# Performance work log

Hardware: AMD Instinct MI355X
Metric: run time of the kernel (lower is better)

Reference implementation:

```python
import jax, jax.numpy as jnp
import numpy as np

N_NODES = 200   # sensors
SEQ = 128       # sequence_length == d_model of per-node transformers
BATCH = 256     # transformer treats batch as the attention sequence (2D input)
HEADS = 4
LAYERS = 2
NF = 1          # num_features (forced to 1 by fc dims)
F_OUT = 64      # num_out_features
G_OUT = 64      # gnn_output_dim
N_EDGES = 1600
D = SEQ
EPS = 1e-5


def setup_inputs() -> dict:
    key = jax.random.key(0)
    ks = jax.random.split(key, 20)
    s = 0.05
    nrm = lambda k, shp: jax.random.normal(k, shp, jnp.float32) * s
    return {
        "x": jax.random.normal(ks[0], (BATCH, N_NODES, SEQ), jnp.float32),
        "edge_index": jax.random.randint(ks[1], (2, N_EDGES), 0, N_NODES),
        # per-node, per-layer transformer params (stacked for vmap)
        "Wqkv": nrm(ks[2], (N_NODES, LAYERS, 3 * D, D)),
        "bqkv": nrm(ks[3], (N_NODES, LAYERS, 3 * D)),
        "Wo": nrm(ks[4], (N_NODES, LAYERS, D, D)),
        "bo": nrm(ks[5], (N_NODES, LAYERS, D)),
        "g1": jnp.ones((N_NODES, LAYERS, D), jnp.float32),
        "be1": jnp.zeros((N_NODES, LAYERS, D), jnp.float32),
        "fW1": nrm(ks[6], (N_NODES, LAYERS, D, D)),  # dim_feedforward = SEQ = D
        "fb1": nrm(ks[7], (N_NODES, LAYERS, D)),
        "fW2": nrm(ks[8], (N_NODES, LAYERS, D, D)),
        "fb2": nrm(ks[9], (N_NODES, LAYERS, D)),
        "g2": jnp.ones((N_NODES, LAYERS, D), jnp.float32),
        "be2": jnp.zeros((N_NODES, LAYERS, D), jnp.float32),
        # shared fc: Linear(SEQ*NF, F_OUT)
        "fc_W": nrm(ks[10], (F_OUT, SEQ * NF)),
        "fc_b": nrm(ks[11], (F_OUT,)),
        # GATConv(F_OUT, G_OUT), heads=1
        "gat_W": nrm(ks[12], (G_OUT, F_OUT)),
        "att_src": nrm(ks[13], (G_OUT,)),
        "att_dst": nrm(ks[14], (G_OUT,)),
        "gat_b": nrm(ks[15], (G_OUT,)),
        # predictor Linear(G_OUT, 2)
        "pred_W": nrm(ks[16], (2, G_OUT)),
        "pred_b": nrm(ks[17], (2,)),
    }


def _ln(v, g, b):
    m = v.mean(-1, keepdims=True)
    var = ((v - m) ** 2).mean(-1, keepdims=True)
    return (v - m) / jnp.sqrt(var + EPS) * g + b


def _encoder_one_node(xn, Wqkv, bqkv, Wo, bo, g1, be1, fW1, fb1, fW2, fb2, g2, be2):
    # xn: [S, D] with S = BATCH (torch treats the 2D input as unbatched seq)
    dh = D // HEADS
    scale = jnp.asarray(1.0 / np.sqrt(dh), xn.dtype)
    for l in range(LAYERS):  # post-norm TransformerEncoderLayer, relu, no dropout (eval)
        qkv = xn @ Wqkv[l].T + bqkv[l]                    # [S, 3D]
        q, k, v = jnp.split(qkv, 3, axis=-1)
        q = q.reshape(-1, HEADS, dh)
        k = k.reshape(-1, HEADS, dh)
        v = v.reshape(-1, HEADS, dh)
        s = jnp.einsum('qhd,khd->hqk', q, k) * scale      # [H, S, S]
        a = jax.nn.softmax(s, axis=-1)
        o = jnp.einsum('hqk,khd->qhd', a, v).reshape(-1, D)
        o = o @ Wo[l].T + bo[l]
        xn = _ln(xn + o, g1[l], be1[l])
        f = jax.nn.relu(xn @ fW1[l].T + fb1[l]) @ fW2[l].T + fb2[l]
        xn = _ln(xn + f, g2[l], be2[l])
    return xn


def _forward(edge_index, x, Wqkv, bqkv, Wo, bo, g1, be1, fW1, fb1, fW2, fb2, g2, be2,
             fc_W, fc_b, gat_W, att_src, att_dst, gat_b, pred_W, pred_b):
    B, N, _ = x.shape
    xt = jnp.transpose(x, (1, 0, 2))                      # [N, B, D]
    t_out = jax.vmap(_encoder_one_node)(xt, Wqkv, bqkv, Wo, bo, g1, be1,
                                        fW1, fb1, fW2, fb2, g2, be2)  # [N, B, D]
    feat = t_out @ fc_W.T + fc_b                          # [N, B, F_OUT]
    # replicate torch.cat(dim=0) over nodes followed by .view(B, N, F)
    feat = feat.reshape(N * B, F_OUT).reshape(B, N, F_OUT)

    # GATConv with add_self_loops, heads=1, negative_slope=0.2
    loops = jnp.arange(N, dtype=edge_index.dtype)
    src = jnp.concatenate([edge_index[0], loops])
    dst = jnp.concatenate([edge_index[1], loops])

    def gat(h_in):  # h_in: [N, F_OUT]
        h = h_in @ gat_W.T                                # [N, G_OUT]
        a_s = h @ att_src                                 # [N]
        a_d = h @ att_dst
        e = jax.nn.leaky_relu(a_s[src] + a_d[dst], 0.2)   # [E+N]
        emax = jax.ops.segment_max(e, dst, num_segments=N)
        emax = jnp.where(jnp.isfinite(emax), emax, 0.0)
        w = jnp.exp(e - emax[dst])
        denom = jax.ops.segment_sum(w, dst, num_segments=N)
        alpha = w / (denom[dst] + 1e-16)
        return jax.ops.segment_sum(alpha[:, None] * h[src], dst, num_segments=N) + gat_b

    g = jax.vmap(gat)(feat)                               # [B, N, G_OUT]
    return g @ pred_W.T + pred_b                          # [B, N, 2]


def reference(x, edge_index, Wqkv, bqkv, Wo, bo, g1, be1, fW1, fb1, fW2, fb2, g2, be2,
              fc_W, fc_b, gat_W, att_src, att_dst, gat_b, pred_W, pred_b):
    return _forward(edge_index, x, Wqkv, bqkv, Wo, bo, g1, be1, fW1, fb1, fW2, fb2,
                    g2, be2, fc_W, fc_b, gat_W, att_src, att_dst, gat_b, pred_W, pred_b)
```

## Files before the change

### kernel.cpp

```cpp
#include <hip/hip_runtime.h>
#include <hip/hip_bf16.h>

#define NN 200
#define BB 256
#define DD 128
#define DH 32
#define NE 1600
#define LL 2

typedef short short8 __attribute__((ext_vector_type(8)));
typedef short short4a __attribute__((ext_vector_type(4)));
typedef float floatx4 __attribute__((ext_vector_type(4)));
using bf16 = __hip_bfloat16;

__device__ __forceinline__ short bfs(float x) {
  bf16 h = __float2bfloat16(x);
  return *(short*)&h;
}
__device__ __forceinline__ float b2f(short s) {
  union { unsigned u; float f; } cv;
  cv.u = ((unsigned)(unsigned short)s) << 16;
  return cv.f;
}

__device__ __forceinline__ void swz_node(int bid, int per_node, int& node, int& rem) {
  int xcd = bid & 7;
  int slot = bid >> 3;
  int q = slot / per_node;
  node = xcd * (NN >> 3) + q;
  rem = slot - q * per_node;
}

__device__ __forceinline__ void ldw_regs(const float* __restrict__ wbase, int tid,
                                         float4* vr) {
#pragma unroll
  for (int i = 0; i < 8; i++) vr[i] = *(const float4*)(wbase + (i * 256 + tid) * 4);
}
__device__ __forceinline__ void st_ws(const float4* vr, short* WS, int tid) {
#pragma unroll
  for (int i = 0; i < 8; i++) {
    int idx = i * 256 + tid;
    int rw = idx >> 5, k = (idx & 31) << 2;
    short4a p = {bfs(vr[i].x), bfs(vr[i].y), bfs(vr[i].z), bfs(vr[i].w)};
    *(short4a*)&WS[rw * 136 + k] = p;
  }
}
__device__ __forceinline__ void stage_w(const float* __restrict__ wbase,
                                        short* WS, int tid) {
  float4 vr[8];
  ldw_regs(wbase, tid, vr);
  st_ws(vr, WS, tid);
}

__device__ __forceinline__ void gemm_q(const short8* af, const short* WS, int r,
                                       int quad, floatx4* acc) {
#pragma unroll
  for (int k0 = 0; k0 < 4; k0++) {
#pragma unroll
    for (int s = 0; s < 4; s++) {
      short8 bq = *(const short8*)&WS[(s * 16 + r) * 136 + quad * 8 + k0 * 32];
      acc[s] = __builtin_amdgcn_mfma_f32_16x16x32_bf16(af[k0], bq, acc[s], 0, 0, 0);
    }
  }
}

__global__ __launch_bounds__(256) void k_transpose(const float* __restrict__ x,
                                                   bf16* __restrict__ X) {
  int tid = blockIdx.x * 256 + threadIdx.x;
  if (tid >= NN * BB * DD) return;
  int d = tid & (DD - 1);
  int rest = tid >> 7;
  int b = rest & (BB - 1);
  int node = rest >> 8;
  X[tid] = (bf16)x[((size_t)b * NN + node) * DD + d];
}

template <int MTPW>
__global__ __launch_bounds__(256) void k_gemm64(const bf16* __restrict__ A,
                                                const float* __restrict__ W,
                                                const float* __restrict__ bias,
                                                bf16* __restrict__ out, int nout,
                                                int astride, size_t woff, int wns,
                                                size_t boff, int bns, int relu,
                                                int nc_count) {
  __shared__ short WS[64 * 136];
  const int RSPLIT = 4 / MTPW;
  int per_node = nc_count * RSPLIT;
  int node, rem;
  swz_node(blockIdx.x, per_node, node, rem);
  int nc = rem / RSPLIT;
  int rh = rem - nc * RSPLIT;
  int tid = threadIdx.x;
  int w = tid >> 6, lane = tid & 63, r = lane & 15, quad = lane >> 4;
  int base_row = rh * 128 + w * (MTPW * 16);

  short8 areg[MTPW][4];
#pragma unroll
  for (int mt = 0; mt < MTPW; mt++) {
    const bf16* arow =
        A + ((size_t)node * BB + base_row + mt * 16 + r) * (size_t)astride + quad * 8;
#pragma unroll
    for (int k = 0; k < 4; k++) areg[mt][k] = *(const short8*)(arow + k * 32);
  }

  stage_w(W + woff + (size_t)node * (size_t)wns + (size_t)nc * 64 * DD, WS, tid);
  __syncthreads();

  floatx4 acc[MTPW][4];
  floatx4 z = {0.f, 0.f, 0.f, 0.f};
#pragma unroll
  for (int mt = 0; mt < MTPW; mt++)
#pragma unroll
    for (int s = 0; s < 4; s++) acc[mt][s] = z;

#pragma unroll
  for (int k0 = 0; k0 < 4; k0++) {
    short8 bq[4];
#pragma unroll
    for (int s = 0; s < 4; s++)
      bq[s] = *(const short8*)&WS[(s * 16 + r) * 136 + quad * 8 + k0 * 32];
#pragma unroll
    for (int mt = 0; mt < MTPW; mt++)
#pragma unroll
      for (int s = 0; s < 4; s++)
        acc[mt][s] = __builtin_amdgcn_mfma_f32_16x16x32_bf16(areg[mt][k0], bq[s],
                                                             acc[mt][s], 0, 0, 0);
  }

  const float* bp = bias + boff + (size_t)node * (size_t)bns + nc * 64;
  float bv[4];
#pragma unroll
  for (int s = 0; s < 4; s++) bv[s] = bp[s * 16 + r];

  __syncthreads();
  short* mybw = &WS[w * 1088];
  const size_t obase = (size_t)node * BB + base_row;
#pragma unroll
  for (int mt = 0; mt < MTPW; mt++) {
#pragma unroll
    for (int s = 0; s < 4; s++) {
#pragma unroll
      for (int i = 0; i < 4; i++) {
        float v = acc[mt][s][i] + bv[s];
        if (relu) v = v > 0.f ? v : 0.f;
        mybw[(quad * 4 + i) * 68 + s * 16 + r] = bfs(v);
      }
    }
#pragma unroll
    for (int j = 0; j < 2; j++) {
      int chunk = j * 64 + lane;
      int rowr = chunk >> 3, c8 = chunk & 7;
      short8 o = *(const short8*)&mybw[rowr * 68 + c8 * 8];
      *(short8*)((short*)out + (obase + mt * 16 + rowr) * (size_t)nout + nc * 64 + c8 * 8) = o;
    }
  }
}

__global__ __launch_bounds__(256) void k_ffn(const bf16* __restrict__ QKV,
                                             const float* __restrict__ Wo,
                                             const float* __restrict__ bo,
                                             bf16* __restrict__ X,
                                             const float* __restrict__ g1,
                                             const float* __restrict__ be1,
                                             const float* __restrict__ fW1,
                                             const float* __restrict__ fb1,
                                             const float* __restrict__ fW2,
                                             const float* __restrict__ fb2,
                                             const float* __restrict__ g2,
                                             const float* __restrict__ be2,
                                             size_t wso, int wns, size_t bso, int bns,
                                             int gstride,
                                             const float* __restrict__ W4,
                                             const float* __restrict__ C4,
                                             float* __restrict__ AS,
                                             float* __restrict__ ADv,
                                             float* __restrict__ HW0,
                                             float* __restrict__ HW1,
                                             int dofinal) {
  __shared__ short WS[64 * 136];
  __shared__ short HB[64 * 136];
  __shared__ short FB[64 * 136];
  int node, bt;
  swz_node(blockIdx.x, 4, node, bt);
  int tid = threadIdx.x;
  int w = tid >> 6, lane = tid & 63, r = lane & 15, quad = lane >> 4;
  int rrow = lane >> 2, cg = lane & 3;
  int row0 = bt * 64 + w * 16;

  const short* qrow = (const short*)QKV + ((size_t)node * BB + row0 + r) * 384 + quad * 8;
  short8 af[4];
#pragma unroll
  for (int k0 = 0; k0 < 4; k0++) af[k0] = *(const short8*)(qrow + k0 * 32);
  size_t xoff = ((size_t)node * BB + row0 + rrow) * DD + cg * 32;
  short8 xres[4];
#pragma unroll
  for (int c = 0; c < 4; c++) xres[c] = *(const short8*)((const short*)X + xoff + c * 8);

  const float* WoN = Wo + wso + (size_t)node * (size_t)wns;
  const float* W1N = fW1 + wso + (size_t)node * (size_t)wns;
  const float* W2N = fW2 + wso + (size_t)node * (size_t)wns;

  floatx4 z = {0.f, 0.f, 0.f, 0.f};
  floatx4 acc[8];
  float vv[32];
  float bv[8];
  float4 wreg[8];

  ldw_regs(WoN, tid, wreg);
  st_ws(wreg, WS, tid);
  __syncthreads();
  ldw_regs(WoN + 64 * DD, tid, wreg);
#pragma unroll
  for (int s = 0; s < 8; s++) acc[s] = z;
  gemm_q(af, WS, r, quad, &acc[0]);
  __syncthreads();
  st_ws(wreg, WS, tid);
  __syncthreads();
  ldw_regs(W1N, tid, wreg);
  gemm_q(af, WS, r, quad, &acc[4]);

  const float* bpo = bo + bso + (size_t)node * (size_t)bns;
#pragma unroll
  for (int cch = 0; cch < 2; cch++)
#pragma unroll
    for (int s = 0; s < 4; s++) bv[cch * 4 + s] = bpo[cch * 64 + s * 16 + r];

  {
    float* BNC = (float*)&HB[w * 16 * 136];
#pragma unroll
    for (int s = 0; s < 4; s++)
#pragma unroll
      for (int i = 0; i < 4; i++)
        BNC[(quad * 4 + i) * 68 + s * 16 + r] = acc[s][i] + bv[s];
    if (cg < 2) {
#pragma unroll
      for (int j = 0; j < 8; j++) {
        float4 t4 = *(const float4*)&BNC[rrow * 68 + (cg & 1) * 32 + j * 4];
        vv[j * 4 + 0] = t4.x; vv[j * 4 + 1] = t4.y;
        vv[j * 4 + 2] = t4.z; vv[j * 4 + 3] = t4.w;
      }
    }
#pragma unroll
    for (int s = 0; s < 4; s++)
#pragma unroll
      for (int i = 0; i < 4; i++)
        BNC[(quad * 4 + i) * 68 + s * 16 + r] = acc[4 + s][i] + bv[4 + s];
    if (cg >= 2) {
#pragma unroll
      for (int j = 0; j < 8; j++) {
        float4 t4 = *(const float4*)&BNC[rrow * 68 + (cg & 1) * 32 + j * 4];
        vv[j * 4 + 0] = t4.x; vv[j * 4 + 1] = t4.y;
        vv[j * 4 + 2] = t4.z; vv[j * 4 + 3] = t4.w;
      }
    }
  }

  float sum = 0.f;
#pragma unroll
  for (int c = 0; c < 4; c++)
#pragma unroll
    for (int j = 0; j < 8; j++) {
      vv[c * 8 + j] += b2f(xres[c][j]);
      sum += vv[c * 8 + j];
    }
  sum += __shfl_xor(sum, 1);
  sum += __shfl_xor(sum, 2);
  float mean = sum * (1.0f / 128.0f);
  float vs = 0.f;
#pragma unroll
  for (int j = 0; j < 32; j++) {
    float d = vv[j] - mean;
    vs += d * d;
  }
  vs += __shfl_xor(vs, 1);
  vs += __shfl_xor(vs, 2);
  float inv = rsqrtf(vs * (1.0f / 128.0f) + 1e-5f);
  {
    const float* gp = g1 + bso + (size_t)node * gstride + cg * 32;
    const float* bep = be1 + bso + (size_t)node * gstride + cg * 32;
#pragma unroll
    for (int c = 0; c < 8; c++) {
      float4 g4 = *(const float4*)(gp + c * 4);
      float4 b4 = *(const float4*)(bep + c * 4);
      vv[c * 4 + 0] = (vv[c * 4 + 0] - mean) * inv * g4.x + b4.x;
      vv[c * 4 + 1] = (vv[c * 4 + 1] - mean) * inv * g4.y + b4.y;
      vv[c * 4 + 2] = (vv[c * 4 + 2] - mean) * inv * g4.z + b4.z;
      vv[c * 4 + 3] = (vv[c * 4 + 3] - mean) * inv * g4.w + b4.w;
    }
  }
  {
    short* hrow = &HB[(w * 16 + rrow) * 136 + cg * 32];
#pragma unroll
    for (int c = 0; c < 4; c++) {
      short8 hs;
#pragma unroll
      for (int j = 0; j < 8; j++) hs[j] = bfs(vv[c * 8 + j]);
      *(short8*)(hrow + c * 8) = hs;
    }
  }

  __syncthreads();
  st_ws(wreg, WS, tid);
  __syncthreads();
  ldw_regs(W1N + 64 * DD, tid, wreg);
  short8 hf[4];
#pragma unroll
  for (int k0 = 0; k0 < 4; k0++)
    hf[k0] = *(const short8*)&HB[(w * 16 + r) * 136 + quad * 8 + k0 * 32];
#pragma unroll
  for (int s = 0; s < 8; s++) acc[s] = z;
  gemm_q(hf, WS, r, quad, &acc[0]);
  __syncthreads();
  st_ws(wreg, WS, tid);
  __syncthreads();
  ldw_regs(W2N, tid, wreg);
  gemm_q(hf, WS, r, quad, &acc[4]);
  {
    const float* bp1 = fb1 + bso + (size_t)node * (size_t)bns;
#pragma unroll
    for (int cch = 0; cch < 2; cch++)
#pragma unroll
      for (int s = 0; s < 4; s++) {
        float bb = bp1[cch * 64 + s * 16 + r];
#pragma unroll
        for (int i = 0; i < 4; i++) {
          float v2 = acc[cch * 4 + s][i] + bb;
          FB[(w * 16 + quad * 4 + i) * 136 + cch * 64 + s * 16 + r] =
              bfs(v2 > 0.f ? v2 : 0.f);
        }
      }
  }

  __syncthreads();
  st_ws(wreg, WS, tid);
  __syncthreads();
  ldw_regs(W2N + 64 * DD, tid, wreg);
  short8 ff[4];
#pragma unroll
  for (int k0 = 0; k0 < 4; k0++)
    ff[k0] = *(const short8*)&FB[(w * 16 + r) * 136 + quad * 8 + k0 * 32];
#pragma unroll
  for (int s = 0; s < 8; s++) acc[s] = z;
  gemm_q(ff, WS, r, quad, &acc[0]);
  __syncthreads();
  st_ws(wreg, WS, tid);
  __syncthreads();
  gemm_q(ff, WS, r, quad, &acc[4]);

  const float* bp2 = fb2 + bso + (size_t)node * (size_t)bns;
#pragma unroll
  for (int cch = 0; cch < 2; cch++)
#pragma unroll
    for (int s = 0; s < 4; s++) bv[cch * 4 + s] = bp2[cch * 64 + s * 16 + r];

  {
    float* BNC = (float*)&FB[w * 16 * 136];
#pragma unroll
    for (int s = 0; s < 4; s++)
#pragma unroll
      for (int i = 0; i < 4; i++)
        BNC[(quad * 4 + i) * 68 + s * 16 + r] = acc[s][i] + bv[s];
    if (cg < 2) {
#pragma unroll
      for (int j = 0; j < 8; j++) {
        float4 t4 = *(const float4*)&BNC[rrow * 68 + (cg & 1) * 32 + j * 4];
        vv[j * 4 + 0] = t4.x; vv[j * 4 + 1] = t4.y;
        vv[j * 4 + 2] = t4.z; vv[j * 4 + 3] = t4.w;
      }
    }
#pragma unroll
    for (int s = 0; s < 4; s++)
#pragma unroll
      for (int i = 0; i < 4; i++)
        BNC[(quad * 4 + i) * 68 + s * 16 + r] = acc[4 + s][i] + bv[4 + s];
    if (cg >= 2) {
#pragma unroll
      for (int j = 0; j < 8; j++) {
        float4 t4 = *(const float4*)&BNC[rrow * 68 + (cg & 1) * 32 + j * 4];
        vv[j * 4 + 0] = t4.x; vv[j * 4 + 1] = t4.y;
        vv[j * 4 + 2] = t4.z; vv[j * 4 + 3] = t4.w;
      }
    }
  }

  sum = 0.f;
#pragma unroll
  for (int c = 0; c < 4; c++) {
    short8 hs = *(const short8*)&HB[(w * 16 + rrow) * 136 + cg * 32 + c * 8];
#pragma unroll
    for (int j = 0; j < 8; j++) {
      vv[c * 8 + j] += b2f(hs[j]);
      sum += vv[c * 8 + j];
    }
  }
  sum += __shfl_xor(sum, 1);
  sum += __shfl_xor(sum, 2);
  mean = sum * (1.0f / 128.0f);
  vs = 0.f;
#pragma unroll
  for (int j = 0; j < 32; j++) {
    float d = vv[j] - mean;
    vs += d * d;
  }
  vs += __shfl_xor(vs, 1);
  vs += __shfl_xor(vs, 2);
  inv = rsqrtf(vs * (1.0f / 128.0f) + 1e-5f);
  {
    const float* gp = g2 + bso + (size_t)node * gstride + cg * 32;
    const float* bep = be2 + bso + (size_t)node * gstride + cg * 32;
#pragma unroll
    for (int c = 0; c < 8; c++) {
      float4 g4 = *(const float4*)(gp + c * 4);
      float4 b4 = *(const float4*)(bep + c * 4);
      vv[c * 4 + 0] = (vv[c * 4 + 0] - mean) * inv * g4.x + b4.x;
      vv[c * 4 + 1] = (vv[c * 4 + 1] - mean) * inv * g4.y + b4.y;
      vv[c * 4 + 2] = (vv[c * 4 + 2] - mean) * inv * g4.z + b4.z;
      vv[c * 4 + 3] = (vv[c * 4 + 3] - mean) * inv * g4.w + b4.w;
    }
  }

  if (!dofinal) {
#pragma unroll
    for (int c = 0; c < 4; c++) {
      short8 os;
#pragma unroll
      for (int j = 0; j < 8; j++) os[j] = bfs(vv[c * 8 + j]);
      *(short8*)((short*)X + xoff + c * 8) = os;
    }
  } else {
    float a0 = 0.f, a1 = 0.f, a2 = 0.f, a3 = 0.f;
#pragma unroll
    for (int c = 0; c < 8; c++) {
      float4 w0 = *(const float4*)(W4 + cg * 32 + c * 4);
      float4 w1 = *(const float4*)(W4 + 128 + cg * 32 + c * 4);
      float4 w2 = *(const float4*)(W4 + 256 + cg * 32 + c * 4);
      float4 w3 = *(const float4*)(W4 + 384 + cg * 32 + c * 4);
      a0 += vv[c * 4] * w0.x + vv[c * 4 + 1] * w0.y + vv[c * 4 + 2] * w0.z + vv[c * 4 + 3] * w0.w;
      a1 += vv[c * 4] * w1.x + vv[c * 4 + 1] * w1.y + vv[c * 4 + 2] * w1.z + vv[c * 4 + 3] * w1.w;
      a2 += vv[c * 4] * w2.x + vv[c * 4 + 1] * w2.y + vv[c * 4 + 2] * w2.z + vv[c * 4 + 3] * w2.w;
      a3 += vv[c * 4] * w3.x + vv[c * 4 + 1] * w3.y + vv[c * 4 + 2] * w3.z + vv[c * 4 + 3] * w3.w;
    }
    a0 += __shfl_xor(a0, 1); a0 += __shfl_xor(a0, 2);
    a1 += __shfl_xor(a1, 1); a1 += __shfl_xor(a1, 2);
    a2 += __shfl_xor(a2, 1); a2 += __shfl_xor(a2, 2);
    a3 += __shfl_xor(a3, 1); a3 += __shfl_xor(a3, 2);
    if (cg == 0) {
      int grow = node * BB + row0 + rrow;
      AS[grow] = a0 + C4[0];
      ADv[grow] = a1 + C4[1];
      HW0[grow] = a2 + C4[2];
      HW1[grow] = a3 + C4[3];
    }
  }
}

__global__ __launch_bounds__(256) void k_attn(bf16* __restrict__ QKV) {
  __shared__ short VT[32 * 264];
  __shared__ short Pw[4 * 2560];
  int node, h;
  swz_node(blockIdx.x, 4, node, h);
  int tid = threadIdx.x;
  int wave = tid >> 6, lane = tid & 63, quad = lane >> 4, l15 = lane & 15;
  short* sbase = (short*)(QKV + (size_t)node * BB * 384);

  int q0 = wave * 64;
  short8 qf[4];
#pragma unroll
  for (int qt = 0; qt < 4; qt++)
    qf[qt] = *(const short8*)(sbase + (size_t)(q0 + qt * 16 + l15) * 384 + h * 32 + quad * 8);

#pragma unroll
  for (int it = 0; it < 4; it++) {
    int i = it * 256 + tid;
    int key = i >> 2, dq = (i & 3) << 3;
    short8 v8 = *(const short8*)(sbase + (size_t)key * 384 + 256 + h * 32 + dq);
#pragma unroll
    for (int j = 0; j < 8; j++) VT[(dq + j) * 264 + key] = v8[j];
  }
  __syncthreads();

  floatx4 zz = {0.f, 0.f, 0.f, 0.f};
  floatx4 acc[2][4];
#pragma unroll
  for (int dt = 0; dt < 2; dt++)
#pragma unroll
    for (int qt = 0; qt < 4; qt++) acc[dt][qt] = zz;
  float lp[4] = {0.f, 0.f, 0.f, 0.f};
  const float scale = 0.17677669529663689f;
  short* mypw = &Pw[wave * 2560];

#define KADDR(kt) (const short8*)(sbase + (size_t)((kt) * 16 + l15) * 384 + 128 + h * 32 + quad * 8)
  short8 kfA = *KADDR(0);
  short8 kfB = *KADDR(1);

  for (int g = 0; g < 8; g++) {
    short8 vf0 = *(const short8*)(&VT[l15 * 264 + g * 32 + quad * 8]);
    short8 vf1 = *(const short8*)(&VT[(16 + l15) * 264 + g * 32 + quad * 8]);
    short8 nA = kfA, nB = kfB;
    if (g < 7) {
      nA = *KADDR(g * 2 + 2);
      nB = *KADDR(g * 2 + 3);
    }
#pragma unroll
    for (int sub = 0; sub < 2; sub++) {
      short8 kf = sub ? kfB : kfA;
#pragma unroll
      for (int qt = 0; qt < 4; qt++) {
        floatx4 st = __builtin_amdgcn_mfma_f32_16x16x32_bf16(kf, qf[qt], zz, 0, 0, 0);
        float e0 = __expf(st[0] * scale);
        float e1 = __expf(st[1] * scale);
        float e2 = __expf(st[2] * scale);
        float e3 = __expf(st[3] * scale);
        lp[qt] += (e0 + e1) + (e2 + e3);
        short4a p = {bfs(e0), bfs(e1), bfs(e2), bfs(e3)};
        *(short4a*)(mypw + qt * 640 + l15 * 40 + sub * 16 + quad * 4) = p;
      }
    }
#pragma unroll
    for (int qt = 0; qt < 4; qt++) {
      short8 pf = *(const short8*)(mypw + qt * 640 + l15 * 40 + quad * 8);
      acc[0][qt] = __builtin_amdgcn_mfma_f32_16x16x32_bf16(vf0, pf, acc[0][qt], 0, 0, 0);
      acc[1][qt] = __builtin_amdgcn_mfma_f32_16x16x32_bf16(vf1, pf, acc[1][qt], 0, 0, 0);
    }
    kfA = nA;
    kfB = nB;
  }
#undef KADDR

  float inv[4];
#pragma unroll
  for (int qt = 0; qt < 4; qt++) {
    float lq = lp[qt];
    lq += __shfl_xor(lq, 16);
    lq += __shfl_xor(lq, 32);
    inv[qt] = 1.0f / lq;
  }

#pragma unroll
  for (int qt = 0; qt < 4; qt++)
#pragma unroll
    for (int dt = 0; dt < 2; dt++)
#pragma unroll
      for (int i = 0; i < 4; i++)
        mypw[(qt * 16 + l15) * 40 + dt * 16 + quad * 4 + i] = bfs(acc[dt][qt][i] * inv[qt]);

#pragma unroll
  for (int r = 0; r < 4; r++) {
    int chunk = r * 64 + lane;
    int query = chunk >> 2, d8 = (chunk & 3) * 8;
    short8 o = *(const short8*)(mypw + query * 40 + d8);
    *(short8*)(sbase + (size_t)(q0 + query) * 384 + h * 32 + d8) = o;
  }
}

__global__ __launch_bounds__(256) void k_prep(const float* __restrict__ gatW,
                                              const float* __restrict__ attS,
                                              const float* __restrict__ attD,
                                              const float* __restrict__ predW,
                                              const float* __restrict__ fcW,
                                              const float* __restrict__ fcb,
                                              float* __restrict__ W4,
                                              float* __restrict__ C4) {
  __shared__ float U[4][64];
  int t = threadIdx.x;
  int tt = t >> 6, f = t & 63;
  float u = 0.f;
  if (tt == 0) {
    for (int g = 0; g < 64; g++) u += gatW[g * 64 + f] * attS[g];
  } else if (tt == 1) {
    for (int g = 0; g < 64; g++) u += gatW[g * 64 + f] * attD[g];
  } else if (tt == 2) {
    for (int g = 0; g < 64; g++) u += gatW[g * 64 + f] * predW[g];
  } else {
    for (int g = 0; g < 64; g++) u += gatW[g * 64 + f] * predW[64 + g];
  }
  U[tt][f] = u;
  __syncthreads();
  for (int idx = t; idx < 512; idx += 256) {
    int v = idx >> 7, d = idx & 127;
    float w = 0.f;
#pragma unroll
    for (int ff = 0; ff < 64; ff++) w += fcW[ff * 128 + d] * U[v][ff];
    W4[v * 128 + d] = w;
  }
  if (t < 4) {
    float c = 0.f;
#pragma unroll
    for (int ff = 0; ff < 64; ff++) c += fcb[ff] * U[t][ff];
    C4[t] = c;
  }
}

__global__ __launch_bounds__(256) void k_gat(const int* __restrict__ EI,
                                             const float* __restrict__ AS,
                                             const float* __restrict__ ADv,
                                             const float* __restrict__ HW0,
                                             const float* __restrict__ HW1,
                                             const float* __restrict__ gatB,
                                             const float* __restrict__ predW,
                                             const float* __restrict__ predB,
                                             float* __restrict__ OUT) {
  __shared__ float sAS[NN], sAD[NN], sH0[NN], sH1[NN];
  __shared__ float n0[NN], n1[NN], den[NN];
  __shared__ float cc[2];
  int b = blockIdx.x;
  int t = threadIdx.x;
  int base = b * NN;
  for (int i = t; i < NN; i += 256) {
    sAS[i] = AS[base + i];
    sAD[i] = ADv[base + i];
    sH0[i] = HW0[base + i];
    sH1[i] = HW1[base + i];
    n0[i] = 0.f;
    n1[i] = 0.f;
    den[i] = 0.f;
  }
  if (t < 64) {
    float p0 = gatB[t] * predW[t];
    float p1 = gatB[t] * predW[64 + t];
#pragma unroll
    for (int off = 32; off; off >>= 1) {
      p0 += __shfl_down(p0, off);
      p1 += __shfl_down(p1, off);
    }
    if (t == 0) {
      cc[0] = p0 + predB[0];
      cc[1] = p1 + predB[1];
    }
  }
  __syncthreads();

  for (int i = t; i < NE + NN; i += 256) {
    int s, d;
    if (i < NE) {
      s = EI[i];
      d = EI[NE + i];
    } else {
      s = d = i - NE;
    }
    float ev = sAS[s] + sAD[d];
    float lr = ev > 0.f ? ev : 0.2f * ev;
    float w = __expf(lr);
    atomicAdd(&n0[d], w * sH0[s]);
    atomicAdd(&n1[d], w * sH1[s]);
    atomicAdd(&den[d], w);
  }
  __syncthreads();

  for (int i = t; i < NN; i += 256) {
    float inv = 1.0f / (den[i] + 1e-16f);
    OUT[2 * (base + i)] = n0[i] * inv + cc[0];
    OUT[2 * (base + i) + 1] = n1[i] * inv + cc[1];
  }
}

extern "C" void kernel_launch(void* const* d_in, const int* in_sizes, int n_in,
                              void* d_out, int out_size, void* d_ws, size_t ws_size,
                              hipStream_t stream) {
  const float* x = (const float*)d_in[0];
  const int* ei = (const int*)d_in[1];
  const float* Wqkv = (const float*)d_in[2];
  const float* bqkv = (const float*)d_in[3];
  const float* Wo = (const float*)d_in[4];
  const float* bo = (const float*)d_in[5];
  const float* g1 = (const float*)d_in[6];
  const float* be1 = (const float*)d_in[7];
  const float* fW1 = (const float*)d_in[8];
  const float* fb1 = (const float*)d_in[9];
  const float* fW2 = (const float*)d_in[10];
  const float* fb2 = (const float*)d_in[11];
  const float* g2 = (const float*)d_in[12];
  const float* be2 = (const float*)d_in[13];
  const float* fcW = (const float*)d_in[14];
  const float* fcb = (const float*)d_in[15];
  const float* gatW = (const float*)d_in[16];
  const float* attS = (const float*)d_in[17];
  const float* attD = (const float*)d_in[18];
  const float* gatB = (const float*)d_in[19];
  const float* predW = (const float*)d_in[20];
  const float* predB = (const float*)d_in[21];

  const size_t NEED = 53477376;
  if (ws_size < NEED) return;

  char* ws = (char*)d_ws;
  bf16* X = (bf16*)(ws);
  bf16* QKV = (bf16*)(ws + 13107200);
  float* W4 = (float*)(ws + 52428800);
  float* C4 = (float*)(ws + 52430848);
  float* AS = (float*)(ws + 52431872);
  float* ADv = (float*)(ws + 52636672);
  float* HW0 = (float*)(ws + 52841472);
  float* HW1 = (float*)(ws + 53046272);

  k_prep<<<1, 256, 0, stream>>>(gatW, attS, attD, predW, fcW, fcb, W4, C4);
  k_transpose<<<25600, 256, 0, stream>>>(x, X);

  for (int l = 0; l < LL; l++) {
    size_t w3o = (size_t)l * 384 * DD, b3o = (size_t)l * 384;
    size_t wso = (size_t)l * DD * DD, bso = (size_t)l * DD;
    k_gemm64<4><<<6 * NN, 256, 0, stream>>>(X, Wqkv, bqkv, QKV, 384, DD,
                                            w3o, LL * 384 * DD, b3o, LL * 384, 0, 6);
    k_attn<<<NN * 4, 256, 0, stream>>>(QKV);
    k_ffn<<<4 * NN, 256, 0, stream>>>(QKV, Wo, bo, X, g1, be1, fW1, fb1, fW2, fb2,
                                      g2, be2, wso, LL * DD * DD, bso, LL * DD,
                                      LL * DD, W4, C4, AS, ADv, HW0, HW1,
                                      (l == LL - 1) ? 1 : 0);
  }

  k_gat<<<BB, 256, 0, stream>>>(ei, AS, ADv, HW0, HW1, gatB, predW, predB,
                                (float*)d_out);
}
```

Before: 402.8 us.

## Fuse input transpose into first-layer GEMM and FFN loads; retune LDS padding

Drops the separate transpose/bf16-conversion kernel. The first layer's QKV GEMM and the FFN residual load now read the fp32 input directly in its original layout and convert to bf16 in registers. This removes one full pass that wrote and reread an intermediate bf16 copy. It also changes the LDS row padding from 136 to 132 shorts and the fp32 staging stride from 68 to 66. That alters bank-conflict behaviour and 16-byte alignment of the vector LDS accesses.

```diff
diff --git a/kernel.cpp b/kernel.cpp
--- a/kernel.cpp
+++ b/kernel.cpp
@@ -31,6 +31,8 @@
   rem = slot - q * per_node;
 }
 
+#define WSTR 132
+
 __device__ __forceinline__ void ldw_regs(const float* __restrict__ wbase, int tid,
                                          float4* vr) {
 #pragma unroll
@@ -42,7 +44,7 @@
     int idx = i * 256 + tid;
     int rw = idx >> 5, k = (idx & 31) << 2;
     short4a p = {bfs(vr[i].x), bfs(vr[i].y), bfs(vr[i].z), bfs(vr[i].w)};
-    *(short4a*)&WS[rw * 136 + k] = p;
+    *(short4a*)&WS[rw * WSTR + k] = p;
   }
 }
 __device__ __forceinline__ void stage_w(const float* __restrict__ wbase,
@@ -58,32 +60,23 @@
   for (int k0 = 0; k0 < 4; k0++) {
 #pragma unroll
     for (int s = 0; s < 4; s++) {
-      short8 bq = *(const short8*)&WS[(s * 16 + r) * 136 + quad * 8 + k0 * 32];
+      short8 bq = *(const short8*)&WS[(s * 16 + r) * WSTR + quad * 8 + k0 * 32];
       acc[s] = __builtin_amdgcn_mfma_f32_16x16x32_bf16(af[k0], bq, acc[s], 0, 0, 0);
     }
   }
-}
-
-__global__ __launch_bounds__(256) void k_transpose(const float* __restrict__ x,
-                                                   bf16* __restrict__ X) {
-  int tid = blockIdx.x * 256 + threadIdx.x;
-  if (tid >= NN * BB * DD) return;
-  int d = tid & (DD - 1);
-  int rest = tid >> 7;
-  int b = rest & (BB - 1);
-  int node = rest >> 8;
-  X[tid] = (bf16)x[((size_t)b * NN + node) * DD + d];
 }
 
 template <int MTPW>
 __global__ __launch_bounds__(256) void k_gemm64(const bf16* __restrict__ A,
+                                                const float* __restrict__ xsrc,
+                                                int xdirect,
                                                 const float* __restrict__ W,
                                                 const float* __restrict__ bias,
                                                 bf16* __restrict__ out, int nout,
                                                 int astride, size_t woff, int wns,
                                                 size_t boff, int bns, int relu,
                                                 int nc_count) {
-  __shared__ short WS[64 * 136];
+  __shared__ short WS[64 * WSTR];
   const int RSPLIT = 4 / MTPW;
   int per_node = nc_count * RSPLIT;
   int node, rem;
@@ -95,12 +88,28 @@
   int base_row = rh * 128 + w * (MTPW * 16);
 
   short8 areg[MTPW][4];
-#pragma unroll
-  for (int mt = 0; mt < MTPW; mt++) {
-    const bf16* arow =
-        A + ((size_t)node * BB + base_row + mt * 16 + r) * (size_t)astride + quad * 8;
-#pragma unroll
-    for (int k = 0; k < 4; k++) areg[mt][k] = *(const short8*)(arow + k * 32);
+  if (xdirect) {
+#pragma unroll
+    for (int mt = 0; mt < MTPW; mt++) {
+      const float* xrow =
+          xsrc + ((size_t)(base_row + mt * 16 + r) * NN + node) * DD + quad * 8;
+#pragma unroll
+      for (int k = 0; k < 4; k++) {
+        float4 a = *(const float4*)(xrow + k * 32);
+        float4 b = *(const float4*)(xrow + k * 32 + 4);
+        short8 v = {bfs(a.x), bfs(a.y), bfs(a.z), bfs(a.w),
+                    bfs(b.x), bfs(b.y), bfs(b.z), bfs(b.w)};
+        areg[mt][k] = v;
+      }
+    }
+  } else {
+#pragma unroll
+    for (int mt = 0; mt < MTPW; mt++) {
+      const bf16* arow =
+          A + ((size_t)node * BB + base_row + mt * 16 + r) * (size_t)astride + quad * 8;
+#pragma unroll
+      for (int k = 0; k < 4; k++) areg[mt][k] = *(const short8*)(arow + k * 32);
+    }
   }
 
   stage_w(W + woff + (size_t)node * (size_t)wns + (size_t)nc * 64 * DD, WS, tid);
@@ -118,7 +127,7 @@
     short8 bq[4];
 #pragma unroll
     for (int s = 0; s < 4; s++)
-      bq[s] = *(const short8*)&WS[(s * 16 + r) * 136 + quad * 8 + k0 * 32];
+      bq[s] = *(const short8*)&WS[(s * 16 + r) * WSTR + quad * 8 + k0 * 32];
 #pragma unroll
     for (int mt = 0; mt < MTPW; mt++)
 #pragma unroll
@@ -133,7 +142,7 @@
   for (int s = 0; s < 4; s++) bv[s] = bp[s * 16 + r];
 
   __syncthreads();
-  short* mybw = &WS[w * 1088];
+  short* mybw = &WS[w * 2112];
   const size_t obase = (size_t)node * BB + base_row;
 #pragma unroll
   for (int mt = 0; mt < MTPW; mt++) {
@@ -157,6 +166,7 @@
 }
 
 __global__ __launch_bounds__(256) void k_ffn(const bf16* __restrict__ QKV,
+                                             const float* __restrict__ xf32,
                                              const float* __restrict__ Wo,
                                              const float* __restrict__ bo,
                                              bf16* __restrict__ X,
@@ -177,9 +187,9 @@
                                              float* __restrict__ HW0,
                                              float* __restrict__ HW1,
                                              int dofinal) {
-  __shared__ short WS[64 * 136];
-  __shared__ short HB[64 * 136];
-  __shared__ short FB[64 * 136];
+  __shared__ short WS[64 * WSTR];
+  __shared__ short HB[64 * WSTR];
+  __shared__ short FB[64 * WSTR];
   int node, bt;
   swz_node(blockIdx.x, 4, node, bt);
   int tid = threadIdx.x;
@@ -193,8 +203,21 @@
   for (int k0 = 0; k0 < 4; k0++) af[k0] = *(const short8*)(qrow + k0 * 32);
   size_t xoff = ((size_t)node * BB + row0 + rrow) * DD + cg * 32;
   short8 xres[4];
-#pragma unroll
-  for (int c = 0; c < 4; c++) xres[c] = *(const short8*)((const short*)X + xoff + c * 8);
+  if (xf32) {
+    const float* xr32 = xf32 + ((size_t)(row0 + rrow) * NN + node) * DD + cg * 32;
+#pragma unroll
+    for (int c = 0; c < 4; c++) {
+      float4 a = *(const float4*)(xr32 + c * 8);
+      float4 b = *(const float4*)(xr32 + c * 8 + 4);
+      short8 v = {bfs(a.x), bfs(a.y), bfs(a.z), bfs(a.w),
+                  bfs(b.x), bfs(b.y), bfs(b.z), bfs(b.w)};
+      xres[c] = v;
+    }
+  } else {
+#pragma unroll
+    for (int c = 0; c < 4; c++)
+      xres[c] = *(const short8*)((const short*)X + xoff + c * 8);
+  }
 
   const float* WoN = Wo + wso + (size_t)node * (size_t)wns;
   const float* W1N = fW1 + wso + (size_t)node * (size_t)wns;
@@ -226,16 +249,16 @@
     for (int s = 0; s < 4; s++) bv[cch * 4 + s] = bpo[cch * 64 + s * 16 + r];
 
   {
-    float* BNC = (float*)&HB[w * 16 * 136];
+    float* BNC = (float*)&HB[w * 2112];
 #pragma unroll
     for (int s = 0; s < 4; s++)
 #pragma unroll
       for (int i = 0; i < 4; i++)
-        BNC[(quad * 4 + i) * 68 + s * 16 + r] = acc[s][i] + bv[s];
+        BNC[(quad * 4 + i) * 66 + s * 16 + r] = acc[s][i] + bv[s];
     if (cg < 2) {
 #pragma unroll
       for (int j = 0; j < 8; j++) {
-        float4 t4 = *(const float4*)&BNC[rrow * 68 + (cg & 1) * 32 + j * 4];
+        float4 t4 = *(const float4*)&BNC[rrow * 66 + (cg & 1) * 32 + j * 4];
         vv[j * 4 + 0] = t4.x; vv[j * 4 + 1] = t4.y;
         vv[j * 4 + 2] = t4.z; vv[j * 4 + 3] = t4.w;
       }
@@ -244,11 +267,11 @@
     for (int s = 0; s < 4; s++)
 #pragma unroll
       for (int i = 0; i < 4; i++)
-        BNC[(quad * 4 + i) * 68 + s * 16 + r] = acc[4 + s][i] + bv[4 + s];
+        BNC[(quad * 4 + i) * 66 + s * 16 + r] = acc[4 + s][i] + bv[4 + s];
     if (cg >= 2) {
 #pragma unroll
       for (int j = 0; j < 8; j++) {
-        float4 t4 = *(const float4*)&BNC[rrow * 68 + (cg & 1) * 32 + j * 4];
+        float4 t4 = *(const float4*)&BNC[rrow * 66 + (cg & 1) * 32 + j * 4];
         vv[j * 4 + 0] = t4.x; vv[j * 4 + 1] = t4.y;
         vv[j * 4 + 2] = t4.z; vv[j * 4 + 3] = t4.w;
       }
@@ -289,7 +312,7 @@
     }
   }
   {
-    short* hrow = &HB[(w * 16 + rrow) * 136 + cg * 32];
+    short* hrow = &HB[(w * 16 + rrow) * WSTR + cg * 32];
 #pragma unroll
     for (int c = 0; c < 4; c++) {
       short8 hs;
@@ -306,7 +329,7 @@
   short8 hf[4];
 #pragma unroll
   for (int k0 = 0; k0 < 4; k0++)
-    hf[k0] = *(const short8*)&HB[(w * 16 + r) * 136 + quad * 8 + k0 * 32];
+    hf[k0] = *(const short8*)&HB[(w * 16 + r) * WSTR + quad * 8 + k0 * 32];
 #pragma unroll
   for (int s = 0; s < 8; s++) acc[s] = z;
   gemm_q(hf, WS, r, quad, &acc[0]);
@@ -325,7 +348,7 @@
 #pragma unroll
         for (int i = 0; i < 4; i++) {
           float v2 = acc[cch * 4 + s][i] + bb;
-          FB[(w * 16 + quad * 4 + i) * 136 + cch * 64 + s * 16 + r] =
+          FB[(w * 16 + quad * 4 + i) * WSTR + cch * 64 + s * 16 + r] =
               bfs(v2 > 0.f ? v2 : 0.f);
         }
       }
@@ -338,7 +361,7 @@
   short8 ff[4];
 #pragma unroll
   for (int k0 = 0; k0 < 4; k0++)
-    ff[k0] = *(const short8*)&FB[(w * 16 + r) * 136 + quad * 8 + k0 * 32];
+    ff[k0] = *(const short8*)&FB[(w * 16 + r) * WSTR + quad * 8 + k0 * 32];
 #pragma unroll
   for (int s = 0; s < 8; s++) acc[s] = z;
   gemm_q(ff, WS, r, quad, &acc[0]);
@@ -354,16 +377,16 @@
     for (int s = 0; s < 4; s++) bv[cch * 4 + s] = bp2[cch * 64 + s * 16 + r];
 
   {
-    float* BNC = (float*)&FB[w * 16 * 136];
+    float* BNC = (float*)&FB[w * 2112];
 #pragma unroll
     for (int s = 0; s < 4; s++)
 #pragma unroll
       for (int i = 0; i < 4; i++)
-        BNC[(quad * 4 + i) * 68 + s * 16 + r] = acc[s][i] + bv[s];
+        BNC[(quad * 4 + i) * 66 + s * 16 + r] = acc[s][i] + bv[s];
     if (cg < 2) {
 #pragma unroll
       for (int j = 0; j < 8; j++) {
-        float4 t4 = *(const float4*)&BNC[rrow * 68 + (cg & 1) * 32 + j * 4];
+        float4 t4 = *(const float4*)&BNC[rrow * 66 + (cg & 1) * 32 + j * 4];
         vv[j * 4 + 0] = t4.x; vv[j * 4 + 1] = t4.y;
         vv[j * 4 + 2] = t4.z; vv[j * 4 + 3] = t4.w;
       }
@@ -372,11 +395,11 @@
     for (int s = 0; s < 4; s++)
 #pragma unroll
       for (int i = 0; i < 4; i++)
-        BNC[(quad * 4 + i) * 68 + s * 16 + r] = acc[4 + s][i] + bv[4 + s];
+        BNC[(quad * 4 + i) * 66 + s * 16 + r] = acc[4 + s][i] + bv[4 + s];
     if (cg >= 2) {
 #pragma unroll
       for (int j = 0; j < 8; j++) {
-        float4 t4 = *(const float4*)&BNC[rrow * 68 + (cg & 1) * 32 + j * 4];
+        float4 t4 = *(const float4*)&BNC[rrow * 66 + (cg & 1) * 32 + j * 4];
         vv[j * 4 + 0] = t4.x; vv[j * 4 + 1] = t4.y;
         vv[j * 4 + 2] = t4.z; vv[j * 4 + 3] = t4.w;
       }
@@ -386,7 +409,7 @@
   sum = 0.f;
 #pragma unroll
   for (int c = 0; c < 4; c++) {
-    short8 hs = *(const short8*)&HB[(w * 16 + rrow) * 136 + cg * 32 + c * 8];
+    short8 hs = *(const short8*)&HB[(w * 16 + rrow) * WSTR + cg * 32 + c * 8];
 #pragma unroll
     for (int j = 0; j < 8; j++) {
       vv[c * 8 + j] += b2f(hs[j]);
@@ -694,17 +717,18 @@
   float* HW1 = (float*)(ws + 53046272);
 
   k_prep<<<1, 256, 0, stream>>>(gatW, attS, attD, predW, fcW, fcb, W4, C4);
-  k_transpose<<<25600, 256, 0, stream>>>(x, X);
 
   for (int l = 0; l < LL; l++) {
     size_t w3o = (size_t)l * 384 * DD, b3o = (size_t)l * 384;
     size_t wso = (size_t)l * DD * DD, bso = (size_t)l * DD;
-    k_gemm64<4><<<6 * NN, 256, 0, stream>>>(X, Wqkv, bqkv, QKV, 384, DD,
-                                            w3o, LL * 384 * DD, b3o, LL * 384, 0, 6);
+    k_gemm64<4><<<6 * NN, 256, 0, stream>>>(X, x, (l == 0) ? 1 : 0, Wqkv, bqkv,
+                                            QKV, 384, DD, w3o, LL * 384 * DD,
+                                            b3o, LL * 384, 0, 6);
     k_attn<<<NN * 4, 256, 0, stream>>>(QKV);
-    k_ffn<<<4 * NN, 256, 0, stream>>>(QKV, Wo, bo, X, g1, be1, fW1, fb1, fW2, fb2,
-                                      g2, be2, wso, LL * DD * DD, bso, LL * DD,
-                                      LL * DD, W4, C4, AS, ADv, HW0, HW1,
+    k_ffn<<<4 * NN, 256, 0, stream>>>(QKV, (l == 0) ? x : nullptr, Wo, bo, X,
+                                      g1, be1, fW1, fb1, fW2, fb2, g2, be2,
+                                      wso, LL * DD * DD, bso, LL * DD, LL * DD,
+                                      W4, C4, AS, ADv, HW0, HW1,
                                       (l == LL - 1) ? 1 : 0);
   }
 
```

Result: slower. 462.3 us (+14.8%).
